# Optimization experiments

Measured on AMD Instinct MI355X. Metric: run time of the kernel, lower is better.

Reference implementation:

```python
import jax, jax.numpy as jnp
import numpy as np

E = 256   # embed_dim
L = 64    # num_landmarks
C = 256   # in_channels
N_ITER = 6


def iterative_inv(K):
    # Newton-Schulz pseudo-inverse on small [*, L, L] matrices (faithful to torch code)
    I = jnp.eye(K.shape[-1], dtype=K.dtype)
    KA = jnp.abs(K)
    V0 = KA.sum(axis=-2, keepdims=True).max(axis=-1, keepdims=True)  # [*,1,1]
    VI = KA.sum(axis=-1, keepdims=True).max(axis=-2, keepdims=True)  # [*,1,1]
    V = jnp.swapaxes(K, -1, -2) / (V0 * VI)
    for _ in range(N_ITER):
        KV = K @ V
        V = 0.25 * V @ (13.0 * I - KV @ (15.0 * I - KV @ (7.0 * I - KV)))
    return V


def setup_inputs() -> dict:
    key = jax.random.key(0)
    k0, k1, k2 = jax.random.split(key, 3)
    x = jax.random.normal(k0, (8, C, 64, 64), dtype=jnp.float32)
    # Conv2d 1x1 weights stored as [out, in]
    w_qkv = jax.random.normal(k1, (3 * E, C), dtype=jnp.float32) * 0.02
    b_qkv = jnp.zeros((3 * E,), dtype=jnp.float32)
    w_out = jax.random.normal(k2, (C, E), dtype=jnp.float32) * 0.02
    b_out = jnp.zeros((C,), dtype=jnp.float32)
    return {"x": x, "w_qkv": w_qkv, "b_qkv": b_qkv, "w_out": w_out, "b_out": b_out}


def reference(x, w_qkv, b_qkv, w_out, b_out):
    N, Cin, H, W = x.shape
    HW = H * W
    # 1x1 conv: [N, 3E, H, W]
    y = jnp.einsum('nchw,ec->nehw', x, w_qkv) + b_qkv[None, :, None, None]
    # faithful raw reshape (mixes channel/spatial like the torch code)
    qkv = y.reshape(N, HW, 3 * E)
    q, k, v = jnp.split(qkv, 3, axis=-1)                     # each [N, HW, E]
    scale = HW ** 0.5
    q_land = q.reshape(N, L, HW // L, E).mean(axis=-2) / scale  # [N, L, E]
    k_land = k.reshape(N, L, HW // L, E).mean(axis=-2) / scale  # [N, L, E]
    # three softmaxes, all over dim=-2 as in the original
    k1 = jax.nn.softmax(jnp.einsum('nie,nje->nij', q, k_land), axis=-2)       # [N, HW, L]
    k2 = jax.nn.softmax(jnp.einsum('nie,nje->nij', q_land, k_land), axis=-2)  # [N, L, L]
    k3 = jax.nn.softmax(jnp.einsum('nie,nje->nij', q_land, k), axis=-2)       # [N, L, HW]
    k2_inv = iterative_inv(k2)
    out = k1 @ (k2_inv @ (k3 @ v)) + v                        # [N, HW, E]
    out = out.reshape(N, E, H, W)                             # faithful raw reshape
    return jnp.einsum('nehw,ce->nchw', out, w_out) + b_out[None, :, None, None]
```

## Files before the change

### kernel.cpp

```cpp
#include <hip/hip_runtime.h>
#include <hip/hip_bf16.h>

typedef unsigned short u16;
typedef __attribute__((ext_vector_type(4))) float f32x4;
typedef __attribute__((ext_vector_type(8))) short short8;

#define NB   8
#define CIN  256
#define EDIM 256
#define M3   768
#define HWN  4096
#define LND  64
#define NS2  72

__device__ __forceinline__ float bf2f(u16 u){ return __uint_as_float(((unsigned)u)<<16); }
__device__ __forceinline__ u16 f2bf(float f){ __hip_bfloat16 h = __float2bfloat16(f); return *reinterpret_cast<u16*>(&h); }
__device__ __forceinline__ void bf2x2(unsigned u, float &lo, float &hi){
  lo = __uint_as_float(u<<16);
  hi = __uint_as_float(u & 0xffff0000u);
}

typedef __attribute__((address_space(1))) unsigned as1_uint;
typedef __attribute__((address_space(3))) unsigned as3_uint;
__device__ __forceinline__ void gl16(const void* g, void* l){
  __builtin_amdgcn_global_load_lds((const as1_uint*)g, (as3_uint*)l, 16, 0, 0);
}

__global__ __launch_bounds__(256) void k_prep(const float* __restrict__ x, u16* __restrict__ Xt,
                                              const float* __restrict__ wq, const float* __restrict__ wo,
                                              u16* __restrict__ Wqb, u16* __restrict__ Wob){
  const int bi = blockIdx.x;
  const int tid = threadIdx.x;
  if(bi >= 2048){
    int ti = (bi-2048)*256 + tid;
    const float* src; u16* dst;
    if(ti < 1536){ src = wq + (size_t)ti*128;        dst = Wqb + (size_t)ti*128; }
    else         { src = wo + (size_t)(ti-1536)*128; dst = Wob + (size_t)(ti-1536)*128; }
    #pragma unroll
    for(int t=0;t<128;t+=8){
      float4 v0 = *(const float4*)(src+t);
      float4 v1 = *(const float4*)(src+t+4);
      ushort4 o0, o1;
      o0.x=f2bf(v0.x); o0.y=f2bf(v0.y); o0.z=f2bf(v0.z); o0.w=f2bf(v0.w);
      o1.x=f2bf(v1.x); o1.y=f2bf(v1.y); o1.z=f2bf(v1.z); o1.w=f2bf(v1.w);
      *(ushort4*)(dst+t)   = o0;
      *(ushort4*)(dst+t+4) = o1;
    }
    return;
  }
  __shared__ float Ts[64*65];
  const int n = bi>>8, rem = bi&255, ct = rem>>6, pt = rem&63;
  const int c0 = ct*64, p0 = pt*64;
  {
    int cc = tid>>2, pj = (tid&3)*16;
    const float* xp = x + (size_t)n*CIN*HWN + (size_t)(c0+cc)*HWN + p0 + pj;
    #pragma unroll
    for(int j=0;j<16;j++) Ts[cc*65 + pj + j] = xp[j];
  }
  __syncthreads();
  {
    int pp = tid>>2, ej = (tid&3)*16;
    u16* op = Xt + ((size_t)n*HWN + p0 + pp)*CIN + c0 + ej;
    ushort4 o[4];
    #pragma unroll
    for(int j=0;j<16;j++) ((u16*)o)[j] = f2bf(Ts[(ej+j)*65 + pp]);
    *(ushort4*)(op+0)  = o[0];
    *(ushort4*)(op+4)  = o[1];
    *(ushort4*)(op+8)  = o[2];
    *(ushort4*)(op+12) = o[3];
  }
}

__global__ __launch_bounds__(256) void k_qkv(const u16* __restrict__ Wb, const u16* __restrict__ Xt,
                                             const float* __restrict__ bias, u16* __restrict__ Y){
  __shared__ __align__(16) u16 As[128*64];
  __shared__ __align__(16) u16 Bs[128*64];
  const int bi = blockIdx.x;
  const int n = bi&7, rem = bi>>3;
  const int ch0 = (rem%6)*128, p0 = (rem/6)*128;
  const int tid = threadIdx.x, lane = tid&63;
  const int c = tid&15, qq = (tid>>4)&3, w4 = tid>>6;
  const int wr0 = (w4&1)*64, wc0 = (w4>>1)*64;
  const u16* xb = Xt + ((size_t)n*HWN + p0)*CIN;
  const u16* wb = Wb + (size_t)ch0*CIN;
  f32x4 acc[4][4];
  #pragma unroll
  for(int mt=0;mt<4;mt++)
    #pragma unroll
    for(int nt=0;nt<4;nt++){ acc[mt][nt][0]=0.f; acc[mt][nt][1]=0.f; acc[mt][nt][2]=0.f; acc[mt][nt][3]=0.f; }
  const int srow  = w4*8 + (lane>>3);
  const int dslot = lane&7;
  const int sgo   = (dslot ^ (lane>>3))*8;
  const int rdswz = (c&7);
  for(int ph=0; ph<4; ph++){
    #pragma unroll
    for(int j=0;j<4;j++){
      int r = j*32 + srow;
      gl16(wb + (size_t)r*CIN + ph*64 + sgo, &As[r*64 + dslot*8]);
    }
    #pragma unroll
    for(int j=0;j<4;j++){
      int r = j*32 + srow;
      gl16(xb + (size_t)r*CIN + ph*64 + sgo, &Bs[r*64 + dslot*8]);
    }
    __syncthreads();
    #pragma unroll
    for(int kt=0;kt<2;kt++){
      short8 af[4], bff[4];
      const int rslot = ((kt*4+qq)^rdswz)*8;
      #pragma unroll
      for(int mt=0;mt<4;mt++) af[mt]  = *(const short8*)&As[(wr0+mt*16+c)*64 + rslot];
      #pragma unroll
      for(int nt=0;nt<4;nt++) bff[nt] = *(const short8*)&Bs[(wc0+nt*16+c)*64 + rslot];
      #pragma unroll
      for(int mt=0;mt<4;mt++)
        #pragma unroll
        for(int nt=0;nt<4;nt++)
          acc[mt][nt] = __builtin_amdgcn_mfma_f32_16x16x32_bf16(af[mt], bff[nt], acc[mt][nt], 0, 0, 0);
    }
    __syncthreads();
  }
  u16* Yb = Y + (size_t)n*M3*HWN;
  #pragma unroll
  for(int mt=0;mt<4;mt++){
    int chb = ch0 + wr0 + mt*16 + 4*qq;
    float b0 = bias[chb], b1 = bias[chb+1], b2 = bias[chb+2], b3 = bias[chb+3];
    #pragma unroll
    for(int nt=0;nt<4;nt++){
      int p = p0 + wc0 + nt*16 + c;
      u16* yp = Yb + (size_t)chb*HWN + p;
      yp[0]             = f2bf(acc[mt][nt][0]+b0);
      yp[HWN]           = f2bf(acc[mt][nt][1]+b1);
      yp[2*(size_t)HWN] = f2bf(acc[mt][nt][2]+b2);
      yp[3*(size_t)HWN] = f2bf(acc[mt][nt][3]+b3);
    }
  }
}

__global__ void k_land(const u16* __restrict__ Y, float* __restrict__ qland, float* __restrict__ kland){
  const int l = blockIdx.x, n = blockIdx.y, e = threadIdx.x;
  const u16* base = Y + (size_t)n*M3*HWN;
  float qs=0.f, ks=0.f;
  #pragma unroll 8
  for(int m=0;m<64;m++){
    size_t off = (size_t)(l*64+m)*M3;
    qs += bf2f(base[off+e]);
    ks += bf2f(base[off+256+e]);
  }
  qland[((size_t)n*LND+l)*EDIM+e] = qs*(1.f/4096.f);
  kland[((size_t)n*LND+l)*EDIM+e] = ks*(1.f/4096.f);
}

__device__ __forceinline__ void ns_mm2(const u16* L, int sL, const u16* Rt, int sR,
                                       int wv, int q, int c, f32x4 r4[4]){
  short8 a0 = *(const short8*)(L + (size_t)(16*wv + c)*sL + 8*q);
  short8 a1 = *(const short8*)(L + (size_t)(16*wv + c)*sL + 32 + 8*q);
  #pragma unroll
  for(int tc=0;tc<4;tc++){
    f32x4 acc = {0.f,0.f,0.f,0.f};
    short8 b0 = *(const short8*)(Rt + (size_t)(16*tc + c)*sR + 8*q);
    short8 b1 = *(const short8*)(Rt + (size_t)(16*tc + c)*sR + 32 + 8*q);
    acc = __builtin_amdgcn_mfma_f32_16x16x32_bf16(a0, b0, acc, 0, 0, 0);
    acc = __builtin_amdgcn_mfma_f32_16x16x32_bf16(a1, b1, acc, 0, 0, 0);
    r4[tc] = acc;
  }
}

#define TTS 64
__device__ void ns_body(int n, char* smem, const float* __restrict__ qland,
                        const float* __restrict__ kland, float* __restrict__ KinvT){
  u16* Kb  = (u16*)(smem + 0);
  u16* Vb  = (u16*)(smem + 9216);
  u16* Vt  = (u16*)(smem + 18432);
  u16* KVb = (u16*)(smem + 27648);
  u16* KVt = (u16*)(smem + 36864);
  u16* Tt  = (u16*)(smem + 46080);
  float* sS   = (float*)(smem + 27648);
  float* sred = (float*)(smem + 44544);
  const int tid = threadIdx.x;
  const int wv = tid>>6, q = (tid>>4)&3, c = tid&15;
  const float* qb = qland + (size_t)n*LND*EDIM;
  const float* kb = kland + (size_t)n*LND*EDIM;
  f32x4 acc[4];
  #pragma unroll
  for(int t=0;t<4;t++){ acc[t][0]=0.f; acc[t][1]=0.f; acc[t][2]=0.f; acc[t][3]=0.f; }
  for(int e0=0;e0<EDIM;e0+=64){
    __syncthreads();
    {
      int row = tid>>2, c0 = (tid&3)*16;
      const float* qp = qb + (size_t)row*EDIM + e0 + c0;
      const float* kp = kb + (size_t)row*EDIM + e0 + c0;
      u16* qd = &KVb[row*NS2 + c0];
      u16* kd = &KVt[row*NS2 + c0];
      #pragma unroll
      for(int j=0;j<16;j+=4){
        float4 qv = *(const float4*)(qp+j);
        float4 kv = *(const float4*)(kp+j);
        ushort4 qo, ko;
        qo.x=f2bf(qv.x); qo.y=f2bf(qv.y); qo.z=f2bf(qv.z); qo.w=f2bf(qv.w);
        ko.x=f2bf(kv.x); ko.y=f2bf(kv.y); ko.z=f2bf(kv.z); ko.w=f2bf(kv.w);
        *(ushort4*)(qd+j) = qo;
        *(ushort4*)(kd+j) = ko;
      }
    }
    __syncthreads();
    {
      short8 a0 = *(const short8*)&KVb[(16*wv+c)*NS2 + 8*q];
      short8 a1 = *(const short8*)&KVb[(16*wv+c)*NS2 + 32 + 8*q];
      #pragma unroll
      for(int tc=0;tc<4;tc++){
        short8 b0 = *(const short8*)&KVt[(16*tc+c)*NS2 + 8*q];
        short8 b1 = *(const short8*)&KVt[(16*tc+c)*NS2 + 32 + 8*q];
        acc[tc] = __builtin_amdgcn_mfma_f32_16x16x32_bf16(a0, b0, acc[tc], 0, 0, 0);
        acc[tc] = __builtin_amdgcn_mfma_f32_16x16x32_bf16(a1, b1, acc[tc], 0, 0, 0);
      }
    }
  }
  __syncthreads();
  #pragma unroll
  for(int tc=0;tc<4;tc++){
    int col = 16*tc + c, row0 = 16*wv + 4*q;
    sS[(row0+0)*66+col] = acc[tc][0];
    sS[(row0+1)*66+col] = acc[tc][1];
    sS[(row0+2)*66+col] = acc[tc][2];
    sS[(row0+3)*66+col] = acc[tc][3];
  }
  __syncthreads();
  if(tid < 64){
    int j = tid;
    float m = -1e30f;
    for(int i=0;i<64;i++) m = fmaxf(m, sS[i*66+j]);
    float ssum = 0.f;
    for(int i=0;i<64;i++) ssum += __expf(sS[i*66+j]-m);
    float inv = 1.f/ssum, cs = 0.f;
    for(int i=0;i<64;i++){
      float kv = __expf(sS[i*66+j]-m)*inv;
      cs += fabsf(kv);
      Kb[i*NS2+j] = f2bf(kv);
    }
    sred[j] = cs;
  }
  __syncthreads();
  if(tid < 64){
    int i = tid; float rs = 0.f;
    for(int j=0;j<64;j++) rs += fabsf(bf2f(Kb[i*NS2+j]));
    sred[64+i] = rs;
  }
  __syncthreads();
  if(tid == 0){
    float v0=-1e30f, vi=-1e30f;
    for(int t=0;t<64;t++){ v0 = fmaxf(v0, sred[t]); vi = fmaxf(vi, sred[64+t]); }
    sred[128] = 1.f/(v0*vi);
  }
  __syncthreads();
  {
    float sc = sred[128];
    int i = tid>>2, j16 = (tid&3)*16;
    #pragma unroll
    for(int jj=0;jj<16;jj++){
      int j = j16+jj;
      u16 bvv = f2bf(bf2f(Kb[j*NS2+i])*sc);
      Vb[i*NS2+j] = bvv;
      Vt[j*NS2+i] = bvv;
    }
  }
  __syncthreads();
  f32x4 r4[4];
  for(int it=0; it<6; it++){
    ns_mm2(Kb, NS2, Vt, NS2, wv, q, c, r4);
    #pragma unroll
    for(int tc=0;tc<4;tc++){
      int col = 16*tc + c, row0 = 16*wv + 4*q;
      ushort4 pk;
      pk.x = f2bf(r4[tc][0]); pk.y = f2bf(r4[tc][1]); pk.z = f2bf(r4[tc][2]); pk.w = f2bf(r4[tc][3]);
      KVb[(row0+0)*NS2+col] = pk.x; KVb[(row0+1)*NS2+col] = pk.y;
      KVb[(row0+2)*NS2+col] = pk.z; KVb[(row0+3)*NS2+col] = pk.w;
      *(ushort4*)&KVt[(size_t)col*NS2 + row0] = pk;
    }
    __syncthreads();
    ns_mm2(KVb, NS2, KVt, NS2, wv, q, c, r4);
    #pragma unroll
    for(int tc=0;tc<4;tc++){
      int col = 16*tc+c, row0 = 16*wv+4*q;
      ushort4 pk;
      #pragma unroll
      for(int r=0;r<4;r++){
        float kvv = bf2f(KVb[(row0+r)*NS2+col]);
        ((u16*)&pk)[r] = f2bf(7.f*kvv - r4[tc][r]);
      }
      *(ushort4*)&Tt[(size_t)col*TTS + row0] = pk;
    }
    __syncthreads();
    ns_mm2(KVb, NS2, Tt, TTS, wv, q, c, r4);
    __syncthreads();
    #pragma unroll
    for(int tc=0;tc<4;tc++){
      int col = 16*tc+c, row0 = 16*wv+4*q;
      ushort4 pk;
      #pragma unroll
      for(int r=0;r<4;r++){
        float kvv = bf2f(KVb[(row0+r)*NS2+col]);
        ((u16*)&pk)[r] = f2bf(15.f*kvv - r4[tc][r]);
      }
      *(ushort4*)&Tt[(size_t)col*TTS + row0] = pk;
    }
    __syncthreads();
    ns_mm2(Vb, NS2, Tt, TTS, wv, q, c, r4);
    __syncthreads();
    #pragma unroll
    for(int tc=0;tc<4;tc++){
      int col = 16*tc+c, row0 = 16*wv+4*q;
      float nv[4]; ushort4 pk;
      #pragma unroll
      for(int r=0;r<4;r++){
        float vv = bf2f(Vb[(row0+r)*NS2+col]);
        nv[r] = 0.25f*(13.f*vv - r4[tc][r]);
        u16 bb = f2bf(nv[r]);
        Vb[(row0+r)*NS2+col] = bb;
        ((u16*)&pk)[r] = bb;
      }
      *(ushort4*)&Vt[(size_t)col*NS2 + row0] = pk;
      if(it==5){
        *(float4*)&KinvT[(size_t)n*4096 + (size_t)col*64 + row0] = make_float4(nv[0],nv[1],nv[2],nv[3]);
      }
    }
    __syncthreads();
  }
}

#define LGS 264
__global__ __launch_bounds__(256) void k_landgemm(const u16* __restrict__ Y, const float* __restrict__ qland,
                                                  const float* __restrict__ kland, float* __restrict__ Z1,
                                                  float* __restrict__ Z3, float* __restrict__ KinvT){
  __shared__ __align__(16) char usm[54272];
  const int z = blockIdx.y;
  if(blockIdx.x == 64){
    if((z&1)==0) ns_body(z>>1, usm, qland, kland, KinvT);
    return;
  }
  u16* As = (u16*)usm;
  u16* BsU = (u16*)(usm + 33792);
  const int n = z>>1, which = z&1;
  const int b0 = blockIdx.x*64;
  const float* land = (which ? qland : kland) + (size_t)n*LND*EDIM;
  const int boff = which ? 256 : 0;
  float* out = (which ? Z3 : Z1) + (size_t)n*LND*HWN;
  const u16* Yb = Y + (size_t)n*M3*HWN + boff;
  const int tid = threadIdx.x, lane = tid&63;
  const int c = tid&15, qq = (tid>>4)&3, wv = tid>>6;
  {
    int r = tid>>2, c0 = (tid&3)*64;
    const float* lp = land + (size_t)r*EDIM + c0;
    u16* dp = &As[r*LGS + c0];
    #pragma unroll
    for(int j=0;j<64;j+=4){
      float4 v = *(const float4*)(lp+j);
      ushort4 o; o.x=f2bf(v.x); o.y=f2bf(v.y); o.z=f2bf(v.z); o.w=f2bf(v.w);
      *(ushort4*)(dp+j) = o;
    }
  }
  const int srow  = wv*8 + (lane>>3);
  const int dslot = lane&7;
  const int sgo   = (dslot ^ (lane>>3))*8;
  const int rdswz = (c&7);
  f32x4 acc[4];
  #pragma unroll
  for(int nt=0;nt<4;nt++){ acc[nt][0]=0.f; acc[nt][1]=0.f; acc[nt][2]=0.f; acc[nt][3]=0.f; }
  #pragma unroll
  for(int j=0;j<2;j++){
    int r = j*32 + srow;
    gl16(Yb + (size_t)(b0+r)*M3 + sgo, BsU + r*64 + dslot*8);
  }
  __syncthreads();
  for(int ph=0; ph<4; ph++){
    const int cur = ph&1;
    if(ph<3){
      #pragma unroll
      for(int j=0;j<2;j++){
        int r = j*32 + srow;
        gl16(Yb + (size_t)(b0+r)*M3 + (ph+1)*64 + sgo, BsU + (cur^1)*4096 + r*64 + dslot*8);
      }
    }
    #pragma unroll
    for(int kt=0;kt<2;kt++){
      short8 af = *(const short8*)&As[(16*wv + c)*LGS + ph*64 + kt*32 + qq*8];
      const int rslot = ((kt*4+qq)^rdswz)*8;
      #pragma unroll
      for(int nt=0;nt<4;nt++){
        short8 bff = *(const short8*)&BsU[cur*4096 + (nt*16+c)*64 + rslot];
        acc[nt] = __builtin_amdgcn_mfma_f32_16x16x32_bf16(af, bff, acc[nt], 0, 0, 0);
      }
    }
    __syncthreads();
  }
  const int m0 = 16*wv + 4*qq;
  #pragma unroll
  for(int nt=0;nt<4;nt++){
    int col = b0 + nt*16 + c;
    out[(size_t)(m0+0)*HWN + col] = acc[nt][0];
    out[(size_t)(m0+1)*HWN + col] = acc[nt][1];
    out[(size_t)(m0+2)*HWN + col] = acc[nt][2];
    out[(size_t)(m0+3)*HWN + col] = acc[nt][3];
  }
}

#define NSTR 76
__device__ void f_body(int idx, char* smem, const float* __restrict__ Z3, const u16* __restrict__ Y,
                       float* __restrict__ part){
  const int kc = idx&31, n = (idx>>5)&7, eh = idx>>8;
  const int tid = threadIdx.x;
  const int jb = kc*128, eb = eh*128;
  float* Sf = (float*)smem;
  u16* k3T  = (u16*)(smem + 33792);
  const float* z3b = Z3 + (size_t)n*LND*HWN;
  {
    int ibase = (tid>>5)*8, j4 = (tid&31)*4;
    #pragma unroll
    for(int r=0;r<8;r++){
      int i = ibase + r;
      *(float4*)&Sf[i*132 + j4] = *(const float4*)&z3b[(size_t)i*HWN + jb + j4];
    }
  }
  __syncthreads();
  if(tid < 128){
    int j = tid;
    float m = -1e30f;
    for(int i=0;i<64;i++) m = fmaxf(m, Sf[i*132 + j]);
    float s = 0.f;
    for(int i=0;i<64;i++){ float e = __expf(Sf[i*132 + j] - m); Sf[i*132 + j] = e; s += e; }
    float inv = 1.f/s;
    u16* kr = &k3T[j*NSTR];
    for(int i=0;i<64;i+=4){
      ushort4 o;
      o.x = f2bf(Sf[(i+0)*132 + j]*inv);
      o.y = f2bf(Sf[(i+1)*132 + j]*inv);
      o.z = f2bf(Sf[(i+2)*132 + j]*inv);
      o.w = f2bf(Sf[(i+3)*132 + j]*inv);
      *(ushort4*)(kr + i) = o;
    }
  }
  __syncthreads();
  const int i0 = (tid>>4)*4, e0 = eb + (tid&15)*8;
  const u16* Yv = Y + (size_t)n*M3*HWN + 512 + e0;
  float acc[4][8] = {};
  uint4 Ub[4]; ushort4 ab[4];
  #pragma unroll
  for(int t=0;t<4;t++){
    ab[t] = *(const ushort4*)&k3T[(size_t)t*NSTR + i0];
    Ub[t] = *(const uint4*)(Yv + (size_t)(jb+t)*M3);
  }
  for(int j0=0;j0<128;j0+=4){
    uint4 Un[4]; ushort4 an[4];
    if(j0 < 124){
      #pragma unroll
      for(int t=0;t<4;t++){
        an[t] = *(const ushort4*)&k3T[(size_t)(j0+4+t)*NSTR + i0];
        Un[t] = *(const uint4*)(Yv + (size_t)(jb+j0+4+t)*M3);
      }
    }
    #pragma unroll
    for(int t=0;t<4;t++){
      float a0 = bf2f(ab[t].x), a1 = bf2f(ab[t].y), a2 = bf2f(ab[t].z), a3 = bf2f(ab[t].w);
      float bv[8];
      bf2x2(Ub[t].x, bv[0], bv[1]);  bf2x2(Ub[t].y, bv[2], bv[3]);
      bf2x2(Ub[t].z, bv[4], bv[5]);  bf2x2(Ub[t].w, bv[6], bv[7]);
      #pragma unroll
      for(int u=0;u<8;u++){
        acc[0][u] += a0*bv[u];
        acc[1][u] += a1*bv[u];
        acc[2][u] += a2*bv[u];
        acc[3][u] += a3*bv[u];
      }
    }
    if(j0 < 124){
      #pragma unroll
      for(int t=0;t<4;t++){ ab[t] = an[t]; Ub[t] = Un[t]; }
    }
  }
  float* pb = part + ((size_t)n*32 + kc)*LND*EDIM;
  #pragma unroll
  for(int s=0;s<4;s++)
    #pragma unroll
    for(int t=0;t<8;t+=4){
      float4 fv = make_float4(acc[s][t],acc[s][t+1],acc[s][t+2],acc[s][t+3]);
      *(float4*)&pb[(size_t)(i0+s)*EDIM + e0 - eb + (eb) + t] = fv;
    }
}

__device__ void soft1_body(int b, char* smem, float* __restrict__ Z1){
  const int n = b>>6, j = b&63, tid = threadIdx.x;
  float* redm = (float*)smem;
  float* reds = redm + 4;
  float* base = Z1 + ((size_t)n*LND + j)*HWN;
  float v[16];
  float m = -1e30f;
  #pragma unroll
  for(int r=0;r<16;r++){ v[r] = base[r*256 + tid]; m = fmaxf(m, v[r]); }
  #pragma unroll
  for(int o=32;o;o>>=1) m = fmaxf(m, __shfl_xor(m, o));
  const int wid = tid>>6;
  if((tid&63)==0) redm[wid] = m;
  __syncthreads();
  m = fmaxf(fmaxf(redm[0],redm[1]), fmaxf(redm[2],redm[3]));
  float s = 0.f;
  #pragma unroll
  for(int r=0;r<16;r++){ v[r] = __expf(v[r]-m); s += v[r]; }
  #pragma unroll
  for(int o=32;o;o>>=1) s += __shfl_xor(s, o);
  if((tid&63)==0) reds[wid] = s;
  __syncthreads();
  s = reds[0]+reds[1]+reds[2]+reds[3];
  float inv = 1.f/s;
  #pragma unroll
  for(int r=0;r<16;r++) base[r*256 + tid] = v[r]*inv;
}

__global__ __launch_bounds__(256) void k_mega(const float* __restrict__ Z3, const u16* __restrict__ Y,
                                              float* __restrict__ part, float* __restrict__ Z1){
  __shared__ __align__(16) char smem[53248];
  const int bi = blockIdx.x;
  if(bi < 512) f_body(bi, smem, Z3, Y, part);
  else         soft1_body(bi-512, smem, Z1);
}

__global__ void k_fred(const float* __restrict__ part, float* __restrict__ B3){
  const int idx = blockIdx.x*256 + threadIdx.x;
  const int n = idx >> 14, rem = idx & 16383;
  const float* p = part + (size_t)n*32*16384 + rem;
  float s = 0.f;
  #pragma unroll
  for(int kc=0;kc<32;kc++) s += p[(size_t)kc*16384];
  B3[idx] = s;
}

__global__ __launch_bounds__(256) void k_c2(const float* __restrict__ KinvT, const float* __restrict__ B3,
                                            float* __restrict__ C2){
  const int eb = blockIdx.x*64, n = blockIdx.y, tid = threadIdx.x;
  __shared__ float KT[64][68];
  __shared__ float Bs2[64][68];
  {
    int l = tid>>2, o16 = (tid&3)*16;
    const float* kp = KinvT + (size_t)n*4096 + l*64 + o16;
    const float* bp = B3 + ((size_t)n*LND + l)*EDIM + eb + o16;
    #pragma unroll
    for(int t=0;t<16;t+=4){
      *(float4*)&KT[l][o16+t]  = *(const float4*)(kp+t);
      *(float4*)&Bs2[l][o16+t] = *(const float4*)(bp+t);
    }
  }
  __syncthreads();
  const int j0 = (tid>>4)*4, u0 = (tid&15)*4;
  float acc[4][4] = {};
  #pragma unroll 8
  for(int l=0;l<64;l++){
    f32x4 a = *(f32x4*)&KT[l][j0];
    f32x4 b = *(f32x4*)&Bs2[l][u0];
    #pragma unroll
    for(int s=0;s<4;s++)
      #pragma unroll
      for(int u=0;u<4;u++) acc[s][u] += a[s]*b[u];
  }
  #pragma unroll
  for(int s=0;s<4;s++){
    float4 fv = make_float4(acc[s][0],acc[s][1],acc[s][2],acc[s][3]);
    *(float4*)&C2[((size_t)n*LND + j0+s)*EDIM + eb + u0] = fv;
  }
}

__global__ __launch_bounds__(256) void k_out(const float* __restrict__ Z1, const float* __restrict__ C2,
                                             const u16* __restrict__ Y, u16* __restrict__ OM){
  const int ib = blockIdx.x*64, n = blockIdx.y, tid = threadIdx.x;
  __shared__ float K1s[64][68];
  __shared__ u16 C2s[64*264];
  {
    int j = tid>>2, i16 = (tid&3)*16;
    const float* zp = Z1 + ((size_t)n*LND + j)*HWN + ib + i16;
    #pragma unroll
    for(int t=0;t<16;t+=4) *(float4*)&K1s[j][i16+t] = *(const float4*)(zp+t);
    int e64 = (tid&3)*64;
    const float* cp = C2 + ((size_t)n*LND + j)*EDIM + e64;
    #pragma unroll
    for(int t=0;t<64;t+=4){
      float4 v = *(const float4*)(cp+t);
      C2s[j*264 + e64+t+0] = f2bf(v.x);
      C2s[j*264 + e64+t+1] = f2bf(v.y);
      C2s[j*264 + e64+t+2] = f2bf(v.z);
      C2s[j*264 + e64+t+3] = f2bf(v.w);
    }
  }
  __syncthreads();
  const int i0 = (tid>>4)*4, e0 = (tid&15)*16;
  float acc[4][16] = {};
  for(int j=0;j<64;j++){
    f32x4 a = *(f32x4*)&K1s[j][i0];
    const u16* cb = &C2s[j*264 + e0];
    uint4 U0 = *(const uint4*)cb;
    uint4 U1 = *(const uint4*)(cb+8);
    float bv[16];
    bf2x2(U0.x, bv[0], bv[1]);  bf2x2(U0.y, bv[2], bv[3]);
    bf2x2(U0.z, bv[4], bv[5]);  bf2x2(U0.w, bv[6], bv[7]);
    bf2x2(U1.x, bv[8], bv[9]);  bf2x2(U1.y, bv[10], bv[11]);
    bf2x2(U1.z, bv[12], bv[13]); bf2x2(U1.w, bv[14], bv[15]);
    #pragma unroll
    for(int u=0;u<16;u++){
      acc[0][u] += a[0]*bv[u];
      acc[1][u] += a[1]*bv[u];
      acc[2][u] += a[2]*bv[u];
      acc[3][u] += a[3]*bv[u];
    }
  }
  const u16* Yb = Y + (size_t)n*M3*HWN;
  u16* ob = OM + (size_t)n*HWN*EDIM;
  #pragma unroll
  for(int s=0;s<4;s++){
    int i = ib + i0 + s;
    const u16* vp = Yb + (size_t)i*M3 + 512 + e0;
    uint4 U0 = *(const uint4*)vp, U1 = *(const uint4*)(vp+8);
    float vv[16];
    bf2x2(U0.x, vv[0], vv[1]);  bf2x2(U0.y, vv[2], vv[3]);
    bf2x2(U0.z, vv[4], vv[5]);  bf2x2(U0.w, vv[6], vv[7]);
    bf2x2(U1.x, vv[8], vv[9]);  bf2x2(U1.y, vv[10], vv[11]);
    bf2x2(U1.z, vv[12], vv[13]); bf2x2(U1.w, vv[14], vv[15]);
    #pragma unroll
    for(int t=0;t<16;t+=4){
      ushort4 o;
      o.x = f2bf(acc[s][t+0]+vv[t+0]);
      o.y = f2bf(acc[s][t+1]+vv[t+1]);
      o.z = f2bf(acc[s][t+2]+vv[t+2]);
      o.w = f2bf(acc[s][t+3]+vv[t+3]);
      *(ushort4*)&ob[(size_t)i*EDIM + e0 + t] = o;
    }
  }
}

__global__ __launch_bounds__(256) void k_trans2(const u16* __restrict__ OM, u16* __restrict__ OMT){
  __shared__ u16 Ts[64*65];
  const int bi = blockIdx.x;
  const int n = bi>>8, rem = bi&255, et = rem>>6, pt = rem&63;
  const int e0 = et*64, p0 = pt*64, tid = threadIdx.x;
  const u16* omb = OM + (size_t)n*HWN*EDIM;
  {
    int ee = tid>>2, pj = (tid&3)*16;
    const u16* ip = omb + (size_t)(e0+ee)*HWN + p0 + pj;
    ushort4 v0 = *(const ushort4*)(ip);
    ushort4 v1 = *(const ushort4*)(ip+4);
    ushort4 v2 = *(const ushort4*)(ip+8);
    ushort4 v3 = *(const ushort4*)(ip+12);
    u16* tp = &Ts[ee*65 + pj];
    tp[0]=v0.x; tp[1]=v0.y; tp[2]=v0.z; tp[3]=v0.w;
    tp[4]=v1.x; tp[5]=v1.y; tp[6]=v1.z; tp[7]=v1.w;
    tp[8]=v2.x; tp[9]=v2.y; tp[10]=v2.z; tp[11]=v2.w;
    tp[12]=v3.x; tp[13]=v3.y; tp[14]=v3.z; tp[15]=v3.w;
  }
  __syncthreads();
  {
    int pp = tid>>2, ej = (tid&3)*16;
    u16* op = OMT + ((size_t)n*HWN + p0 + pp)*EDIM + e0 + ej;
    ushort4 o[4];
    #pragma unroll
    for(int j=0;j<16;j++) ((u16*)o)[j] = Ts[(ej+j)*65 + pp];
    *(ushort4*)(op+0)  = o[0];
    *(ushort4*)(op+4)  = o[1];
    *(ushort4*)(op+8)  = o[2];
    *(ushort4*)(op+12) = o[3];
  }
}

__global__ __launch_bounds__(256) void k_proj(const u16* __restrict__ Wb, const u16* __restrict__ OMT,
                                              const float* __restrict__ bias, float* __restrict__ out){
  __shared__ __align__(16) u16 As[128*64];
  __shared__ __align__(16) u16 Bs[128*64];
  const int bi = blockIdx.x;
  const int n = bi&7, rem = bi>>3;
  const int ch0 = (rem&1)*128, p0 = (rem>>1)*128;
  const int tid = threadIdx.x, lane = tid&63;
  const int c = tid&15, qq = (tid>>4)&3, w4 = tid>>6;
  const int wr0 = (w4&1)*64, wc0 = (w4>>1)*64;
  const u16* xb = OMT + ((size_t)n*HWN + p0)*EDIM;
  const u16* wb = Wb + (size_t)ch0*EDIM;
  f32x4 acc[4][4];
  #pragma unroll
  for(int mt=0;mt<4;mt++)
    #pragma unroll
    for(int nt=0;nt<4;nt++){ acc[mt][nt][0]=0.f; acc[mt][nt][1]=0.f; acc[mt][nt][2]=0.f; acc[mt][nt][3]=0.f; }
  const int srow  = w4*8 + (lane>>3);
  const int dslot = lane&7;
  const int sgo   = (dslot ^ (lane>>3))*8;
  const int rdswz = (c&7);
  for(int ph=0; ph<4; ph++){
    #pragma unroll
    for(int j=0;j<4;j++){
      int r = j*32 + srow;
      gl16(wb + (size_t)r*EDIM + ph*64 + sgo, &As[r*64 + dslot*8]);
    }
    #pragma unroll
    for(int j=0;j<4;j++){
      int r = j*32 + srow;
      gl16(xb + (size_t)r*EDIM + ph*64 + sgo, &Bs[r*64 + dslot*8]);
    }
    __syncthreads();
    #pragma unroll
    for(int kt=0;kt<2;kt++){
      short8 af[4], bff[4];
      const int rslot = ((kt*4+qq)^rdswz)*8;
      #pragma unroll
      for(int mt=0;mt<4;mt++) af[mt]  = *(const short8*)&As[(wr0+mt*16+c)*64 + rslot];
      #pragma unroll
      for(int nt=0;nt<4;nt++) bff[nt] = *(const short8*)&Bs[(wc0+nt*16+c)*64 + rslot];
      #pragma unroll
      for(int mt=0;mt<4;mt++)
        #pragma unroll
        for(int nt=0;nt<4;nt++)
          acc[mt][nt] = __builtin_amdgcn_mfma_f32_16x16x32_bf16(af[mt], bff[nt], acc[mt][nt], 0, 0, 0);
    }
    __syncthreads();
  }
  float* ob = out + (size_t)n*EDIM*HWN;
  #pragma unroll
  for(int mt=0;mt<4;mt++){
    int chb = ch0 + wr0 + mt*16 + 4*qq;
    float b0 = bias[chb], b1 = bias[chb+1], b2 = bias[chb+2], b3 = bias[chb+3];
    #pragma unroll
    for(int nt=0;nt<4;nt++){
      int p = p0 + wc0 + nt*16 + c;
      float* yp = ob + (size_t)chb*HWN + p;
      yp[0]             = acc[mt][nt][0]+b0;
      yp[HWN]           = acc[mt][nt][1]+b1;
      yp[2*(size_t)HWN] = acc[mt][nt][2]+b2;
      yp[3*(size_t)HWN] = acc[mt][nt][3]+b3;
    }
  }
}

extern "C" void kernel_launch(void* const* d_in, const int* in_sizes, int n_in,
                              void* d_out, int out_size, void* d_ws, size_t ws_size,
                              hipStream_t stream){
  (void)out_size; (void)ws_size;
  const float* x     = (const float*)d_in[0];
  const float* w_qkv = (const float*)d_in[1];
  const float* b_qkv = (const float*)d_in[2];
  const float* w_out = (const float*)d_in[3];
  const float* b_out = (const float*)d_in[4];
  for(int i=0;i<n_in;i++){
    switch(in_sizes[i]){
      case 8388608: x     = (const float*)d_in[i]; break;
      case 196608:  w_qkv = (const float*)d_in[i]; break;
      case 768:     b_qkv = (const float*)d_in[i]; break;
      case 65536:   w_out = (const float*)d_in[i]; break;
      case 256:     b_out = (const float*)d_in[i]; break;
      default: break;
    }
  }
  float* out = (float*)d_out;
  char* ws = (char*)d_ws;

  u16*   Y     = (u16*)(ws + 0);
  float* qland = (float*)(ws + 50331648);
  float* kland = (float*)(ws + 50855936);
  float* Z1    = (float*)(ws + 51380224);
  float* Z3    = (float*)(ws + 59768832);
  float* KinvT = (float*)(ws + 68157440);
  u16*   Xt    = (u16*)(ws + 68288512);
  float* part  = (float*)(ws + 68288512);
  u16*   OMT   = (u16*)(ws + 68288512);
  float* B3    = (float*)(ws + 85065728);
  float* C2    = (float*)(ws + 85590016);
  u16*   OM    = (u16*)(ws + 86114304);
  u16*   Wqb   = (u16*)(ws + 59768832);
  u16*   Wob   = (u16*)(ws + 102891520);

  k_prep    <<<dim3(2056),   256, 0, stream>>>(x, Xt, w_qkv, w_out, Wqb, Wob);
  k_qkv     <<<dim3(1536),   256, 0, stream>>>(Wqb, Xt, b_qkv, Y);
  k_land    <<<dim3(64,8),   256, 0, stream>>>(Y, qland, kland);
  k_landgemm<<<dim3(65,16),  256, 0, stream>>>(Y, qland, kland, Z1, Z3, KinvT);
  k_mega    <<<dim3(1024),   256, 0, stream>>>(Z3, Y, part, Z1);
  k_fred    <<<dim3(512),    256, 0, stream>>>(part, B3);
  k_c2      <<<dim3(4,8),    256, 0, stream>>>(KinvT, B3, C2);
  k_out     <<<dim3(64,8),   256, 0, stream>>>(Z1, C2, Y, OM);
  k_trans2  <<<dim3(2048),   256, 0, stream>>>(OM, OMT);
  k_proj    <<<dim3(512),    256, 0, stream>>>(Wob, OMT, b_out, out);
}
```

Baseline: 237.1 us.

## Split k3 softmax from k3@V and compute the product with bf16 MFMA

The fused softmax-plus-FMA kernel is split in two. One kernel writes the column-softmaxed k3 as bf16 to a global buffer. A new kernel then computes the partial k3@V products with 16x16x32 bf16 MFMA instructions, using swizzled LDS tiles and an in-LDS transpose of V. This replaces scalar FP32 FMAs with matrix-core work. The cost is an extra launch and a round trip of the bf16 P buffer through global memory, and the softmax is no longer recomputed for each of the two E-halves.

Result: faster. 220.8 us (-6.8%).

```diff
diff --git a/kernel.cpp b/kernel.cpp
--- a/kernel.cpp
+++ b/kernel.cpp
@@ -404,14 +404,11 @@
   }
 }
 
-#define NSTR 76
-__device__ void f_body(int idx, char* smem, const float* __restrict__ Z3, const u16* __restrict__ Y,
-                       float* __restrict__ part){
-  const int kc = idx&31, n = (idx>>5)&7, eh = idx>>8;
-  const int tid = threadIdx.x;
-  const int jb = kc*128, eb = eh*128;
-  float* Sf = (float*)smem;
-  u16* k3T  = (u16*)(smem + 33792);
+__device__ void soft3_body(int idx, char* smem, const float* __restrict__ Z3, u16* __restrict__ P){
+  const int kc = idx&31, n = idx>>5;
+  const int tid = threadIdx.x, jb = kc*128;
+  float* Sf   = (float*)smem;
+  float* sinv = (float*)(smem + 33792);
   const float* z3b = Z3 + (size_t)n*LND*HWN;
   {
     int ibase = (tid>>5)*8, j4 = (tid&31)*4;
@@ -428,63 +425,22 @@
     for(int i=0;i<64;i++) m = fmaxf(m, Sf[i*132 + j]);
     float s = 0.f;
     for(int i=0;i<64;i++){ float e = __expf(Sf[i*132 + j] - m); Sf[i*132 + j] = e; s += e; }
-    float inv = 1.f/s;
-    u16* kr = &k3T[j*NSTR];
-    for(int i=0;i<64;i+=4){
+    sinv[j] = 1.f/s;
+  }
+  __syncthreads();
+  {
+    int i = tid>>2, j0 = (tid&3)*32;
+    u16* pp = P + ((size_t)n*LND + i)*HWN + jb + j0;
+    #pragma unroll
+    for(int t=0;t<32;t+=4){
       ushort4 o;
-      o.x = f2bf(Sf[(i+0)*132 + j]*inv);
-      o.y = f2bf(Sf[(i+1)*132 + j]*inv);
-      o.z = f2bf(Sf[(i+2)*132 + j]*inv);
-      o.w = f2bf(Sf[(i+3)*132 + j]*inv);
-      *(ushort4*)(kr + i) = o;
-    }
-  }
-  __syncthreads();
-  const int i0 = (tid>>4)*4, e0 = eb + (tid&15)*8;
-  const u16* Yv = Y + (size_t)n*M3*HWN + 512 + e0;
-  float acc[4][8] = {};
-  uint4 Ub[4]; ushort4 ab[4];
-  #pragma unroll
-  for(int t=0;t<4;t++){
-    ab[t] = *(const ushort4*)&k3T[(size_t)t*NSTR + i0];
-    Ub[t] = *(const uint4*)(Yv + (size_t)(jb+t)*M3);
-  }
-  for(int j0=0;j0<128;j0+=4){
-    uint4 Un[4]; ushort4 an[4];
-    if(j0 < 124){
-      #pragma unroll
-      for(int t=0;t<4;t++){
-        an[t] = *(const ushort4*)&k3T[(size_t)(j0+4+t)*NSTR + i0];
-        Un[t] = *(const uint4*)(Yv + (size_t)(jb+j0+4+t)*M3);
-      }
-    }
-    #pragma unroll
-    for(int t=0;t<4;t++){
-      float a0 = bf2f(ab[t].x), a1 = bf2f(ab[t].y), a2 = bf2f(ab[t].z), a3 = bf2f(ab[t].w);
-      float bv[8];
-      bf2x2(Ub[t].x, bv[0], bv[1]);  bf2x2(Ub[t].y, bv[2], bv[3]);
-      bf2x2(Ub[t].z, bv[4], bv[5]);  bf2x2(Ub[t].w, bv[6], bv[7]);
-      #pragma unroll
-      for(int u=0;u<8;u++){
-        acc[0][u] += a0*bv[u];
-        acc[1][u] += a1*bv[u];
-        acc[2][u] += a2*bv[u];
-        acc[3][u] += a3*bv[u];
-      }
-    }
-    if(j0 < 124){
-      #pragma unroll
-      for(int t=0;t<4;t++){ ab[t] = an[t]; Ub[t] = Un[t]; }
-    }
-  }
-  float* pb = part + ((size_t)n*32 + kc)*LND*EDIM;
-  #pragma unroll
-  for(int s=0;s<4;s++)
-    #pragma unroll
-    for(int t=0;t<8;t+=4){
-      float4 fv = make_float4(acc[s][t],acc[s][t+1],acc[s][t+2],acc[s][t+3]);
-      *(float4*)&pb[(size_t)(i0+s)*EDIM + e0 - eb + (eb) + t] = fv;
-    }
+      o.x = f2bf(Sf[i*132 + j0+t+0]*sinv[j0+t+0]);
+      o.y = f2bf(Sf[i*132 + j0+t+1]*sinv[j0+t+1]);
+      o.z = f2bf(Sf[i*132 + j0+t+2]*sinv[j0+t+2]);
+      o.w = f2bf(Sf[i*132 + j0+t+3]*sinv[j0+t+3]);
+      *(ushort4*)(pp+t) = o;
+    }
+  }
 }
 
 __device__ void soft1_body(int b, char* smem, float* __restrict__ Z1){
@@ -515,12 +471,85 @@
   for(int r=0;r<16;r++) base[r*256 + tid] = v[r]*inv;
 }
 
-__global__ __launch_bounds__(256) void k_mega(const float* __restrict__ Z3, const u16* __restrict__ Y,
-                                              float* __restrict__ part, float* __restrict__ Z1){
-  __shared__ __align__(16) char smem[53248];
+__global__ __launch_bounds__(256) void k_mega(const float* __restrict__ Z3, u16* __restrict__ P,
+                                              float* __restrict__ Z1){
+  __shared__ __align__(16) char smem[34304];
   const int bi = blockIdx.x;
-  if(bi < 512) f_body(bi, smem, Z3, Y, part);
-  else         soft1_body(bi-512, smem, Z1);
+  if(bi < 256) soft3_body(bi, smem, Z3, P);
+  else         soft1_body(bi-256, smem, Z1);
+}
+
+__global__ __launch_bounds__(256) void k_pv(const u16* __restrict__ P, const u16* __restrict__ Y,
+                                            float* __restrict__ part){
+  __shared__ __align__(16) u16 As[64*64];
+  __shared__ __align__(16) u16 Vt[128*64];
+  const int bi = blockIdx.x;
+  const int kc = bi&31, n = (bi>>5)&7, eh = bi>>8;
+  const int jb = kc*128, eb = eh*128;
+  const int tid = threadIdx.x, lane = tid&63;
+  const int c = tid&15, qq = (tid>>4)&3, wv = tid>>6;
+  const u16* Pb = P + (size_t)n*LND*HWN;
+  const u16* Yb = Y + (size_t)n*M3*HWN;
+  const int srow  = wv*8 + (lane>>3);
+  const int dslot = lane&7;
+  const int sgo   = (dslot ^ (lane>>3))*8;
+  const int rdswz = (c&7);
+  f32x4 acc[4][2];
+  #pragma unroll
+  for(int mt=0;mt<4;mt++)
+    #pragma unroll
+    for(int nt=0;nt<2;nt++){ acc[mt][nt][0]=0.f; acc[mt][nt][1]=0.f; acc[mt][nt][2]=0.f; acc[mt][nt][3]=0.f; }
+  for(int ph=0; ph<2; ph++){
+    #pragma unroll
+    for(int j=0;j<2;j++){
+      int r = j*32 + srow;
+      gl16(Pb + (size_t)r*HWN + jb + ph*64 + sgo, &As[r*64 + dslot*8]);
+    }
+    #pragma unroll
+    for(int rep=0; rep<4; rep++){
+      int jl = (tid>>4) + 16*rep;
+      int ec = (tid&15)*8;
+      uint4 U = *(const uint4*)&Yb[(size_t)(jb+ph*64+jl)*M3 + 512 + eb + ec];
+      const u16* uv = (const u16*)&U;
+      #pragma unroll
+      for(int k=0;k<8;k++){
+        int e = ec+k;
+        int slot = ((jl>>3) ^ (e&7) ^ ((e>>3)&7)) & 7;
+        Vt[e*64 + slot*8 + (jl&7)] = uv[k];
+      }
+    }
+    __syncthreads();
+    #pragma unroll
+    for(int kt=0;kt<2;kt++){
+      const int rslotA = ((kt*4+qq)^rdswz)*8;
+      short8 af[4];
+      #pragma unroll
+      for(int mt=0;mt<4;mt++) af[mt] = *(const short8*)&As[(mt*16+c)*64 + rslotA];
+      #pragma unroll
+      for(int nt=0;nt<2;nt++){
+        int e = wv*32 + nt*16 + c;
+        int slotB = ((kt*4+qq) ^ (e&7) ^ ((e>>3)&7)) & 7;
+        short8 bf_ = *(const short8*)&Vt[e*64 + slotB*8];
+        #pragma unroll
+        for(int mt=0;mt<4;mt++)
+          acc[mt][nt] = __builtin_amdgcn_mfma_f32_16x16x32_bf16(af[mt], bf_, acc[mt][nt], 0, 0, 0);
+      }
+    }
+    __syncthreads();
+  }
+  float* pb = part + ((size_t)n*32 + kc)*LND*EDIM + eb;
+  #pragma unroll
+  for(int mt=0;mt<4;mt++){
+    int row0 = mt*16 + 4*qq;
+    #pragma unroll
+    for(int nt=0;nt<2;nt++){
+      int e = wv*32 + nt*16 + c;
+      pb[(size_t)(row0+0)*EDIM + e] = acc[mt][nt][0];
+      pb[(size_t)(row0+1)*EDIM + e] = acc[mt][nt][1];
+      pb[(size_t)(row0+2)*EDIM + e] = acc[mt][nt][2];
+      pb[(size_t)(row0+3)*EDIM + e] = acc[mt][nt][3];
+    }
+  }
 }
 
 __global__ void k_fred(const float* __restrict__ part, float* __restrict__ B3){
@@ -766,6 +795,7 @@
   float* B3    = (float*)(ws + 85065728);
   float* C2    = (float*)(ws + 85590016);
   u16*   OM    = (u16*)(ws + 86114304);
+  u16*   Pbuf  = (u16*)(ws + 86114304);
   u16*   Wqb   = (u16*)(ws + 59768832);
   u16*   Wob   = (u16*)(ws + 102891520);
 
@@ -773,7 +803,8 @@
   k_qkv     <<<dim3(1536),   256, 0, stream>>>(Wqb, Xt, b_qkv, Y);
   k_land    <<<dim3(64,8),   256, 0, stream>>>(Y, qland, kland);
   k_landgemm<<<dim3(65,16),  256, 0, stream>>>(Y, qland, kland, Z1, Z3, KinvT);
-  k_mega    <<<dim3(1024),   256, 0, stream>>>(Z3, Y, part, Z1);
+  k_mega    <<<dim3(768),    256, 0, stream>>>(Z3, Pbuf, Z1);
+  k_pv      <<<dim3(512),    256, 0, stream>>>(Pbuf, Y, part);
   k_fred    <<<dim3(512),    256, 0, stream>>>(part, B3);
   k_c2      <<<dim3(4,8),    256, 0, stream>>>(KinvT, B3, C2);
   k_out     <<<dim3(64,8),   256, 0, stream>>>(Z1, C2, Y, OM);
```
